# Performance work log

Measured on AMD Instinct MI355X. Metric: run time of the kernel, lower is better.

## Reference

```python
import jax, jax.numpy as jnp
import numpy as np

B, N, M = 16, 4096, 256
Q_DIM, CTX_DIM = 512, 768
HEADS, DIM_HEAD = 8, 64
INNER = HEADS * DIM_HEAD
SCALE = DIM_HEAD ** -0.5


def setup_inputs() -> dict:
    key = jax.random.key(0)
    ks = jax.random.split(key, 8)
    x = jax.random.normal(ks[0], (B, N, Q_DIM), dtype=jnp.float32)
    obj_txt = jax.random.normal(ks[1], (B, M, CTX_DIM), dtype=jnp.float32)
    obj_mask = jax.random.randint(ks[2], (B, N, M), 0, 2) > 0
    obj_vector = jnp.ones((B, M), dtype=bool)  # all-True keeps output finite (see notes)
    Wq = jax.random.normal(ks[3], (Q_DIM, INNER), dtype=jnp.float32) * 0.02
    Wk = jax.random.normal(ks[4], (CTX_DIM, INNER), dtype=jnp.float32) * 0.02
    Wv = jax.random.normal(ks[5], (CTX_DIM, INNER), dtype=jnp.float32) * 0.02
    Wo = jax.random.normal(ks[6], (INNER, Q_DIM), dtype=jnp.float32) * 0.02
    bo = jnp.zeros((Q_DIM,), dtype=jnp.float32)
    return {"x": x, "obj_txt": obj_txt, "obj_mask": obj_mask, "obj_vector": obj_vector,
            "Wq": Wq, "Wk": Wk, "Wv": Wv, "Wo": Wo, "bo": bo}


def reference(x, obj_txt, obj_mask, obj_vector, Wq, Wk, Wv, Wo, bo):
    b, n, _ = x.shape
    m = obj_txt.shape[1]
    q = (x @ Wq).reshape(b, n, HEADS, DIM_HEAD)          # [B,N,H,C]
    k = (obj_txt @ Wk).reshape(b, m, HEADS, DIM_HEAD)    # [B,M,H,C]
    v = (obj_txt @ Wv).reshape(b, m, HEADS, DIM_HEAD)
    sim = jnp.einsum('bnhc,bmhc->bhnm', q, k) * SCALE    # [B,H,N,M]
    neg = -jnp.finfo(sim.dtype).max
    # pre-softmax mask (obj_vector broadcasts over heads and queries)
    sim = jnp.where(obj_vector[:, None, None, :], sim, neg)
    # NOTE: original computes sim.softmax(-1) but then discards it, using the
    # pre-softmax masked sim with ~obj_mask positions set to 0 as the attention.
    attn = jnp.where(obj_mask[:, None, :, :], sim, jnp.array(0.0, sim.dtype))
    out = jnp.einsum('bhnm,bmhc->bnhc', attn, v).reshape(b, n, INNER)
    return out @ Wo + bo
```

## Files before the change

kernel.cpp:

```cpp
#include <hip/hip_runtime.h>

typedef unsigned short u16;
typedef unsigned char u8;
typedef unsigned int u32;
typedef unsigned long long u64;
typedef __attribute__((ext_vector_type(4))) float floatx4;
typedef __attribute__((ext_vector_type(8))) __bf16 bf16x8;

#define GLD_LDS(SRC, DST) __builtin_amdgcn_global_load_lds( \
    (const __attribute__((address_space(1))) void*)(SRC),   \
    (__attribute__((address_space(3))) void*)(DST), 16, 0, 0)

static __device__ __forceinline__ u16 f2bf(float f) {
  return __builtin_bit_cast(u16, (__bf16)f);
}
static __device__ __forceinline__ u32 pk2bf(float a, float b) {
  return (u32)f2bf(a) | ((u32)f2bf(b) << 16);
}
static __device__ __forceinline__ floatx4 mfma16(bf16x8 a, bf16x8 b, floatx4 c) {
  return __builtin_amdgcn_mfma_f32_16x16x32_bf16(a, b, c, 0, 0, 0);
}


__global__ void detect_mask_kernel(const unsigned int* __restrict__ m, int* __restrict__ flag) {
  __shared__ int sh[4];
  int t = threadIdx.x;
  int any = 0;
  for (int i = t; i < 16384; i += 256) any |= ((m[i] & 0xFFFFFF00u) != 0u) ? 1 : 0;
  unsigned long long b = __ballot(any != 0);
  if ((t & 63) == 0) sh[t >> 6] = (b != 0ull) ? 1 : 0;
  __syncthreads();
  if (t == 0) flag[0] = (sh[0] | sh[1] | sh[2] | sh[3]);
}

__global__ void prep_weights_kernel(const float* __restrict__ Wq, const float* __restrict__ Wk,
                                    const float* __restrict__ Wv, const float* __restrict__ Wo,
                                    u16* __restrict__ WqT, u16* __restrict__ WkT,
                                    u16* __restrict__ WvT, u16* __restrict__ WoT) {
  int z = blockIdx.y;
  const float* src = (z == 0) ? Wq : (z == 1) ? Wk : (z == 2) ? Wv : Wo;
  u16* dst = (z == 0) ? WqT : (z == 1) ? WkT : (z == 2) ? WvT : WoT;
  int K = (z == 1 || z == 2) ? 768 : 512;
  int total = K * 512;
  int idx = blockIdx.x * 256 + threadIdx.x;
  if (idx >= total) return;
  int n = idx / K, k = idx - n * K;
  float v = src[(size_t)k * 512 + n];
  if (z == 0) v *= 0.125f;
  dst[idx] = f2bf(v);
}

__global__ __launch_bounds__(256) void gemm_q_kernel(
    const float* __restrict__ A, const u16* __restrict__ Bt, u16* __restrict__ Cout) {
  __shared__ float Asf[2][4096];
  __shared__ u16 Bs[2][8192];
  int bid = blockIdx.x;
  int m0 = (bid >> 1) * 128, n0 = (bid & 1) * 256;
  int t = threadIdx.x, lane = t & 63;
  int w = t >> 6, wr = w >> 1, wc = w & 1, lr = lane & 15, lg = lane >> 4;
  floatx4 acc[4][8];
#pragma unroll
  for (int i = 0; i < 4; ++i)
#pragma unroll
    for (int j = 0; j < 8; ++j) acc[i][j] = (floatx4){0.f, 0.f, 0.f, 0.f};

  auto stage = [&](int kt, int bf) {
    int k0 = kt * 32;
#pragma unroll
    for (int i = 0; i < 4; ++i) {
      int idx = (i * 4 + w) * 64 + lane;
      int row = idx >> 3, g = idx & 7;
      int gs = g ^ (row & 7);
      const float* src = A + (size_t)(m0 + row) * 512 + k0 + gs * 4;
      char* dst = ((char*)&Asf[0][0]) + bf * 16384 + (i * 4 + w) * 1024;
      GLD_LDS(src, dst);
    }
#pragma unroll
    for (int i = 0; i < 4; ++i) {
      int idx = (i * 4 + w) * 64 + lane;
      int row = idx >> 2, g = idx & 3;
      int gs = g ^ ((row >> 1) & 3);
      const u16* src = Bt + (size_t)(n0 + row) * 512 + k0 + gs * 8;
      char* dst = ((char*)&Bs[0][0]) + bf * 16384 + (i * 4 + w) * 1024;
      GLD_LDS(src, dst);
    }
  };

  stage(0, 0);
  __syncthreads();
  for (int kt = 0; kt < 16; ++kt) {
    int cur = kt & 1;
    if (kt + 1 < 16) stage(kt + 1, cur ^ 1);
    bf16x8 av[4];
#pragma unroll
    for (int i = 0; i < 4; ++i) {
      int r = wr * 64 + i * 16 + lr;
      int g0 = (2 * lg) ^ (r & 7), g1 = (2 * lg + 1) ^ (r & 7);
      float4 f0 = *reinterpret_cast<const float4*>(&Asf[cur][r * 32 + g0 * 4]);
      float4 f1 = *reinterpret_cast<const float4*>(&Asf[cur][r * 32 + g1 * 4]);
      bf16x8 pk;
      pk[0] = (__bf16)f0.x; pk[1] = (__bf16)f0.y; pk[2] = (__bf16)f0.z; pk[3] = (__bf16)f0.w;
      pk[4] = (__bf16)f1.x; pk[5] = (__bf16)f1.y; pk[6] = (__bf16)f1.z; pk[7] = (__bf16)f1.w;
      av[i] = pk;
    }
#pragma unroll
    for (int j = 0; j < 8; ++j) {
      int rb = wc * 128 + j * 16 + lr;
      int gb = lg ^ ((rb >> 1) & 3);
      bf16x8 bv = *reinterpret_cast<const bf16x8*>(&Bs[cur][rb * 32 + gb * 8]);
#pragma unroll
      for (int i = 0; i < 4; ++i) acc[i][j] = mfma16(bv, av[i], acc[i][j]);
    }
    __syncthreads();
  }
#pragma unroll
  for (int i = 0; i < 4; ++i)
#pragma unroll
    for (int j = 0; j < 8; ++j) {
      int n_row = m0 + wr * 64 + i * 16 + lr;
      int colb = n0 + wc * 128 + j * 16 + lg * 4;
      ushort4 pk4;
      pk4.x = f2bf(acc[i][j][0]); pk4.y = f2bf(acc[i][j][1]);
      pk4.z = f2bf(acc[i][j][2]); pk4.w = f2bf(acc[i][j][3]);
      *reinterpret_cast<ushort4*>(&Cout[(size_t)n_row * 512 + colb]) = pk4;
    }
}

__global__ __launch_bounds__(256) void gemm_kv_kernel(
    const float* __restrict__ A, const u16* __restrict__ Bt0, const u16* __restrict__ Bt1,
    u16* __restrict__ C0, u16* __restrict__ C1) {
  const u16* Bt = Bt0;
  u16* Cout = C0;
  int mode = 0;
  if (blockIdx.z == 1) { Bt = Bt1; Cout = C1; mode = 2; }
  __shared__ float Asf[2][4096];
  __shared__ u16 Bs[2][4096];
  int m0 = blockIdx.x * 128, n0 = blockIdx.y * 128;
  int t = threadIdx.x, lane = t & 63;
  int w = t >> 6, wr = w >> 1, wc = w & 1, lr = lane & 15, lg = lane >> 4;
  floatx4 acc[4][4];
#pragma unroll
  for (int i = 0; i < 4; ++i)
#pragma unroll
    for (int j = 0; j < 4; ++j) acc[i][j] = (floatx4){0.f, 0.f, 0.f, 0.f};

  auto stage = [&](int kt, int bf) {
    int k0 = kt * 32;
#pragma unroll
    for (int i = 0; i < 4; ++i) {
      int idx = (i * 4 + w) * 64 + lane;
      int row = idx >> 3, g = idx & 7;
      int gs = g ^ (row & 7);
      const float* src = A + (size_t)(m0 + row) * 768 + k0 + gs * 4;
      char* dst = ((char*)&Asf[0][0]) + bf * 16384 + (i * 4 + w) * 1024;
      GLD_LDS(src, dst);
    }
#pragma unroll
    for (int i = 0; i < 2; ++i) {
      int idx = (i * 4 + w) * 64 + lane;
      int row = idx >> 2, g = idx & 3;
      int gs = g ^ ((row >> 1) & 3);
      const u16* src = Bt + (size_t)(n0 + row) * 768 + k0 + gs * 8;
      char* dst = ((char*)&Bs[0][0]) + bf * 8192 + (i * 4 + w) * 1024;
      GLD_LDS(src, dst);
    }
  };

  stage(0, 0);
  __syncthreads();
  for (int kt = 0; kt < 24; ++kt) {
    int cur = kt & 1;
    if (kt + 1 < 24) stage(kt + 1, cur ^ 1);
    bf16x8 av[4];
#pragma unroll
    for (int i = 0; i < 4; ++i) {
      int r = wr * 64 + i * 16 + lr;
      int g0 = (2 * lg) ^ (r & 7), g1 = (2 * lg + 1) ^ (r & 7);
      float4 f0 = *reinterpret_cast<const float4*>(&Asf[cur][r * 32 + g0 * 4]);
      float4 f1 = *reinterpret_cast<const float4*>(&Asf[cur][r * 32 + g1 * 4]);
      bf16x8 pk;
      pk[0] = (__bf16)f0.x; pk[1] = (__bf16)f0.y; pk[2] = (__bf16)f0.z; pk[3] = (__bf16)f0.w;
      pk[4] = (__bf16)f1.x; pk[5] = (__bf16)f1.y; pk[6] = (__bf16)f1.z; pk[7] = (__bf16)f1.w;
      av[i] = pk;
    }
#pragma unroll
    for (int j = 0; j < 4; ++j) {
      int rb = wc * 64 + j * 16 + lr;
      int gb = lg ^ ((rb >> 1) & 3);
      bf16x8 bv = *reinterpret_cast<const bf16x8*>(&Bs[cur][rb * 32 + gb * 8]);
#pragma unroll
      for (int i = 0; i < 4; ++i) acc[i][j] = mfma16(bv, av[i], acc[i][j]);
    }
    __syncthreads();
  }
#pragma unroll
  for (int i = 0; i < 4; ++i)
#pragma unroll
    for (int j = 0; j < 4; ++j) {
      int n_row = m0 + wr * 64 + i * 16 + lr;
      int colb = n0 + wc * 64 + j * 16 + lg * 4;
      if (mode == 0) {
        ushort4 pk4;
        pk4.x = f2bf(acc[i][j][0]); pk4.y = f2bf(acc[i][j][1]);
        pk4.z = f2bf(acc[i][j][2]); pk4.w = f2bf(acc[i][j][3]);
        *reinterpret_cast<ushort4*>(&Cout[(size_t)n_row * 512 + colb]) = pk4;
      } else {
        int bb = n_row >> 8, mm = n_row & 255;
#pragma unroll
        for (int r = 0; r < 4; ++r) {
          int col = colb + r;
          int hh = col >> 6, cc = col & 63;
          Cout[(((size_t)(bb * 8 + hh)) * 64 + cc) * 256 + mm] = f2bf(acc[i][j][r]);
        }
      }
    }
}

__global__ __launch_bounds__(256) void gemm_o_kernel(
    const u16* __restrict__ A, const u16* __restrict__ Bt, const float* __restrict__ bo,
    float* __restrict__ out) {
  __shared__ u16 As[2][4096];
  __shared__ u16 Bs[2][8192];
  int bid = blockIdx.x;
  int m0 = (bid >> 1) * 128, n0 = (bid & 1) * 256;
  int t = threadIdx.x, lane = t & 63;
  int w = t >> 6, wr = w >> 1, wc = w & 1, lr = lane & 15, lg = lane >> 4;
  floatx4 acc[4][8];
#pragma unroll
  for (int i = 0; i < 4; ++i)
#pragma unroll
    for (int j = 0; j < 8; ++j) acc[i][j] = (floatx4){0.f, 0.f, 0.f, 0.f};

  auto stage = [&](int kt, int bf) {
    int k0 = kt * 32;
#pragma unroll
    for (int i = 0; i < 2; ++i) {
      int idx = (i * 4 + w) * 64 + lane;
      int row = idx >> 2, g = idx & 3;
      int gs = g ^ ((row >> 1) & 3);
      const u16* src = A + (size_t)(m0 + row) * 512 + k0 + gs * 8;
      char* dst = ((char*)&As[0][0]) + bf * 8192 + (i * 4 + w) * 1024;
      GLD_LDS(src, dst);
    }
#pragma unroll
    for (int i = 0; i < 4; ++i) {
      int idx = (i * 4 + w) * 64 + lane;
      int row = idx >> 2, g = idx & 3;
      int gs = g ^ ((row >> 1) & 3);
      const u16* src = Bt + (size_t)(n0 + row) * 512 + k0 + gs * 8;
      char* dst = ((char*)&Bs[0][0]) + bf * 16384 + (i * 4 + w) * 1024;
      GLD_LDS(src, dst);
    }
  };

  stage(0, 0);
  __syncthreads();
  for (int kt = 0; kt < 16; ++kt) {
    int cur = kt & 1;
    if (kt + 1 < 16) stage(kt + 1, cur ^ 1);
    bf16x8 av[4];
#pragma unroll
    for (int i = 0; i < 4; ++i) {
      int r = wr * 64 + i * 16 + lr;
      int ga = lg ^ ((r >> 1) & 3);
      av[i] = *reinterpret_cast<const bf16x8*>(&As[cur][r * 32 + ga * 8]);
    }
#pragma unroll
    for (int j = 0; j < 8; ++j) {
      int rb = wc * 128 + j * 16 + lr;
      int gb = lg ^ ((rb >> 1) & 3);
      bf16x8 bv = *reinterpret_cast<const bf16x8*>(&Bs[cur][rb * 32 + gb * 8]);
#pragma unroll
      for (int i = 0; i < 4; ++i) acc[i][j] = mfma16(bv, av[i], acc[i][j]);
    }
    __syncthreads();
  }
#pragma unroll
  for (int i = 0; i < 4; ++i)
#pragma unroll
    for (int j = 0; j < 8; ++j) {
      int n_row = m0 + wr * 64 + i * 16 + lr;
      int colb = n0 + wc * 128 + j * 16 + lg * 4;
      float4 bv4 = *reinterpret_cast<const float4*>(&bo[colb]);
      float4 st;
      st.x = acc[i][j][0] + bv4.x; st.y = acc[i][j][1] + bv4.y;
      st.z = acc[i][j][2] + bv4.z; st.w = acc[i][j][3] + bv4.w;
      *reinterpret_cast<float4*>(&out[(size_t)n_row * 512 + colb]) = st;
    }
}

__global__ __launch_bounds__(512, 2) void attn_kernel(
    u16* qoin, const u16* __restrict__ Kb, const u16* __restrict__ Vt,
    const void* __restrict__ maskp, const int* __restrict__ flag) {
  __shared__ u16 k_lds[16384];
  __shared__ u16 v_lds[16384];
  __shared__ u16 ubuf[8][1024];
  int id = blockIdx.y * 32 + blockIdx.x;
  int xcd = id & 7, j0 = id >> 3;
  int bIdx = 2 * xcd + (j0 >> 5);
  int nx = j0 & 31;
  int lane = threadIdx.x & 63, w = threadIdx.x >> 6, lr = lane & 15, lg = lane >> 4;
  int n0w = nx * 128 + w * 16;
  bool mByte = flag[0] != 0;

  u64 mb;
  {
    int n = n0w + lr;
    size_t base = ((size_t)(bIdx * 4096 + n)) * 256;
    u64 bits = 0;
    if (mByte) {
      const u8* mp = (const u8*)maskp + base;
      for (int mt = 0; mt < 16; ++mt) {
        u32 dw = *(const u32*)(mp + mt * 16 + lg * 4);
#pragma unroll
        for (int r = 0; r < 4; ++r)
          if ((dw >> (8 * r)) & 0xFFu) bits |= (1ull << (mt * 4 + r));
      }
    } else {
      const int* mp = (const int*)maskp + base;
      for (int mt = 0; mt < 16; ++mt) {
        int4 q = *(const int4*)(mp + mt * 16 + lg * 4);
        if (q.x) bits |= 1ull << (mt * 4 + 0);
        if (q.y) bits |= 1ull << (mt * 4 + 1);
        if (q.z) bits |= 1ull << (mt * 4 + 2);
        if (q.w) bits |= 1ull << (mt * 4 + 3);
      }
    }
    mb = bits;
  }

  for (int h = 0; h < 8; ++h) {
    __syncthreads();
#pragma unroll
    for (int i = 0; i < 4; ++i) {
      int idx = (i * 8 + w) * 64 + lane;
      int m = idx >> 3, g = idx & 7;
      int gs = g ^ (m & 7);
      const u16* src = Kb + ((size_t)(bIdx * 256 + m)) * 512 + h * 64 + gs * 8;
      char* dst = ((char*)k_lds) + (i * 8 + w) * 1024;
      GLD_LDS(src, dst);
    }
#pragma unroll
    for (int i = 0; i < 4; ++i) {
      int idx = (i * 8 + w) * 64 + lane;
      int c = idx >> 5, g = idx & 31;
      int gs = (g & 24) | ((g & 7) ^ (c & 7));
      const u16* src = Vt + (((size_t)(bIdx * 8 + h)) * 64 + c) * 256 + gs * 8;
      char* dst = ((char*)v_lds) + (i * 8 + w) * 1024;
      GLD_LDS(src, dst);
    }
    bf16x8 qf[2];
#pragma unroll
    for (int ks = 0; ks < 2; ++ks)
      qf[ks] = *reinterpret_cast<const bf16x8*>(
          qoin + ((size_t)(bIdx * 4096 + n0w + lr)) * 512 + h * 64 + ks * 32 + lg * 8);
    __syncthreads();

    floatx4 acc2[4];
#pragma unroll
    for (int ct = 0; ct < 4; ++ct) acc2[ct] = (floatx4){0.f, 0.f, 0.f, 0.f};

    for (int ch = 0; ch < 8; ++ch) {
      floatx4 s[2];
#pragma unroll
      for (int mt2 = 0; mt2 < 2; ++mt2) s[mt2] = (floatx4){0.f, 0.f, 0.f, 0.f};
#pragma unroll
      for (int mt2 = 0; mt2 < 2; ++mt2) {
        int m = (ch * 2 + mt2) * 16 + lr;
#pragma unroll
        for (int ks = 0; ks < 2; ++ks) {
          int g = ks * 4 + lg;
          bf16x8 af = *reinterpret_cast<const bf16x8*>(&k_lds[m * 64 + ((g ^ (m & 7)) << 3)]);
          s[mt2] = mfma16(af, qf[ks], s[mt2]);
        }
      }
      u32* pb = (u32*)&ubuf[w][0];
#pragma unroll
      for (int mt2 = 0; mt2 < 2; ++mt2) {
        int sh = (ch * 2 + mt2) * 4;
        float v0 = ((mb >> (sh + 0)) & 1ull) ? s[mt2][0] : 0.f;
        float v1 = ((mb >> (sh + 1)) & 1ull) ? s[mt2][1] : 0.f;
        float v2 = ((mb >> (sh + 2)) & 1ull) ? s[mt2][2] : 0.f;
        float v3 = ((mb >> (sh + 3)) & 1ull) ? s[mt2][3] : 0.f;
        int gm = mt2 * 4 + lg;
        int gmp = gm ^ ((lr & 3) << 1);
        u64 pkd = (u64)pk2bf(v0, v1) | ((u64)pk2bf(v2, v3) << 32);
        *(u64*)(pb + lr * 16 + gmp * 2) = pkd;
      }
      int gmp = (2 * lg) ^ ((lr & 3) << 1);
      bf16x8 pf = *reinterpret_cast<const bf16x8*>(&ubuf[w][lr * 32 + gmp * 4]);
#pragma unroll
      for (int ct = 0; ct < 4; ++ct) {
        int c = ct * 16 + lr;
        int gv = ch * 4 + lg;
        int gvp = (gv & 24) | ((gv & 7) ^ (c & 7));
        bf16x8 vf = *reinterpret_cast<const bf16x8*>(&v_lds[c * 256 + gvp * 8]);
        acc2[ct] = mfma16(pf, vf, acc2[ct]);
      }
    }

#pragma unroll
    for (int ct = 0; ct < 4; ++ct)
#pragma unroll
      for (int r = 0; r < 4; ++r) {
        int c = ct * 16 + lr;
        int n = lg * 4 + r;
        int cg = c >> 3;
        ubuf[w][n * 64 + ((cg ^ (n & 7)) << 3) + (c & 7)] = f2bf(acc2[ct][r]);
      }
#pragma unroll
    for (int half = 0; half < 2; ++half) {
      int np = (lane >> 3) + half * 8;
      int cc = lane & 7;
      bf16x8 frag = *reinterpret_cast<const bf16x8*>(&ubuf[w][np * 64 + ((cc ^ (np & 7)) << 3)]);
      *reinterpret_cast<bf16x8*>(
          qoin + ((size_t)(bIdx * 4096 + n0w + np)) * 512 + h * 64 + cc * 8) = frag;
    }
  }
}

extern "C" void kernel_launch(void* const* d_in, const int* in_sizes, int n_in,
                              void* d_out, int out_size, void* d_ws, size_t ws_size,
                              hipStream_t stream) {
  const float* x = (const float*)d_in[0];
  const float* obj_txt = (const float*)d_in[1];
  const void* obj_mask = d_in[2];
  const float* Wq = (const float*)d_in[4];
  const float* Wk = (const float*)d_in[5];
  const float* Wv = (const float*)d_in[6];
  const float* Wo = (const float*)d_in[7];
  const float* bo = (const float*)d_in[8];
  float* out = (float*)d_out;

  char* ws = (char*)d_ws;
  u16* Qb = (u16*)ws;
  u16* Kb = (u16*)(ws + 67108864);
  u16* Vt = (u16*)(ws + 71303168);
  u16* WqT = (u16*)(ws + 75497472);
  u16* WkT = (u16*)(ws + 76021760);
  u16* WvT = (u16*)(ws + 76808192);
  u16* WoT = (u16*)(ws + 77594624);
  int* flag = (int*)(ws + 78118912);

  detect_mask_kernel<<<1, 256, 0, stream>>>((const unsigned int*)obj_mask, flag);
  prep_weights_kernel<<<dim3(1536, 4, 1), 256, 0, stream>>>(Wq, Wk, Wv, Wo, WqT, WkT, WvT, WoT);
  gemm_q_kernel<<<1024, 256, 0, stream>>>(x, WqT, Qb);
  gemm_kv_kernel<<<dim3(32, 4, 2), 256, 0, stream>>>(obj_txt, WkT, WvT, Kb, Vt);
  attn_kernel<<<dim3(32, 16, 1), 512, 0, stream>>>(Qb, Kb, Vt, obj_mask, flag);
  gemm_o_kernel<<<1024, 256, 0, stream>>>(Qb, WoT, bo, out);
}
```

Baseline: 304.4 us.

## Pre-convert x to bf16 in a separate pass and tile the weight transpose

Adds a kernel that converts x from fp32 to bf16 into the output buffer, which serves as scratch, so the Q GEMM streams half as many bytes into LDS and skips per-tile float-to-bf16 packing. The weight prep kernel now transposes through a padded shared-memory tile so both reads and writes are coalesced. The cost is one extra launch and a full extra read and write pass over x (fp32 in, bf16 out), and gemm_o must fully overwrite the output buffer afterwards.

```diff
diff --git a/kernel.cpp b/kernel.cpp
--- a/kernel.cpp
+++ b/kernel.cpp
@@ -33,26 +33,52 @@
   if (t == 0) flag[0] = (sh[0] | sh[1] | sh[2] | sh[3]);
 }
 
-__global__ void prep_weights_kernel(const float* __restrict__ Wq, const float* __restrict__ Wk,
-                                    const float* __restrict__ Wv, const float* __restrict__ Wo,
-                                    u16* __restrict__ WqT, u16* __restrict__ WkT,
-                                    u16* __restrict__ WvT, u16* __restrict__ WoT) {
+__global__ __launch_bounds__(256) void convert_x_kernel(const float* __restrict__ x,
+                                                        u16* __restrict__ xb) {
+  for (int u = blockIdx.x * 256 + threadIdx.x; u < 4194304; u += 524288) {
+    const float4* p = reinterpret_cast<const float4*>(x + (size_t)u * 8);
+    float4 f0 = p[0], f1 = p[1];
+    bf16x8 pk;
+    pk[0] = (__bf16)f0.x; pk[1] = (__bf16)f0.y; pk[2] = (__bf16)f0.z; pk[3] = (__bf16)f0.w;
+    pk[4] = (__bf16)f1.x; pk[5] = (__bf16)f1.y; pk[6] = (__bf16)f1.z; pk[7] = (__bf16)f1.w;
+    *reinterpret_cast<bf16x8*>(xb + (size_t)u * 8) = pk;
+  }
+}
+
+__global__ __launch_bounds__(256) void prep_weights_kernel(
+    const float* __restrict__ Wq, const float* __restrict__ Wk,
+    const float* __restrict__ Wv, const float* __restrict__ Wo,
+    u16* __restrict__ WqT, u16* __restrict__ WkT,
+    u16* __restrict__ WvT, u16* __restrict__ WoT) {
   int z = blockIdx.y;
   const float* src = (z == 0) ? Wq : (z == 1) ? Wk : (z == 2) ? Wv : Wo;
   u16* dst = (z == 0) ? WqT : (z == 1) ? WkT : (z == 2) ? WvT : WoT;
   int K = (z == 1 || z == 2) ? 768 : 512;
-  int total = K * 512;
-  int idx = blockIdx.x * 256 + threadIdx.x;
-  if (idx >= total) return;
-  int n = idx / K, k = idx - n * K;
-  float v = src[(size_t)k * 512 + n];
-  if (z == 0) v *= 0.125f;
-  dst[idx] = f2bf(v);
+  int nk64 = K >> 6;
+  int tile = blockIdx.x;
+  int kt = tile % nk64, ntile = tile / nk64;
+  if (ntile >= 8) return;
+  int k0 = kt * 64, n0 = ntile * 64;
+  float scale = (z == 0) ? 0.125f : 1.f;
+  __shared__ u16 sh[64 * 65];
+  int t = threadIdx.x;
+#pragma unroll
+  for (int i = 0; i < 16; ++i) {
+    int kk = i * 4 + (t >> 6), nn = t & 63;
+    float v = src[(size_t)(k0 + kk) * 512 + n0 + nn] * scale;
+    sh[kk * 65 + nn] = f2bf(v);
+  }
+  __syncthreads();
+#pragma unroll
+  for (int i = 0; i < 16; ++i) {
+    int nn = i * 4 + (t >> 6), kk = t & 63;
+    dst[(size_t)(n0 + nn) * K + k0 + kk] = sh[kk * 65 + nn];
+  }
 }
 
 __global__ __launch_bounds__(256) void gemm_q_kernel(
-    const float* __restrict__ A, const u16* __restrict__ Bt, u16* __restrict__ Cout) {
-  __shared__ float Asf[2][4096];
+    const u16* __restrict__ A, const u16* __restrict__ Bt, u16* __restrict__ Cout) {
+  __shared__ u16 As[2][4096];
   __shared__ u16 Bs[2][8192];
   int bid = blockIdx.x;
   int m0 = (bid >> 1) * 128, n0 = (bid & 1) * 256;
@@ -67,12 +93,12 @@
   auto stage = [&](int kt, int bf) {
     int k0 = kt * 32;
 #pragma unroll
-    for (int i = 0; i < 4; ++i) {
-      int idx = (i * 4 + w) * 64 + lane;
-      int row = idx >> 3, g = idx & 7;
-      int gs = g ^ (row & 7);
-      const float* src = A + (size_t)(m0 + row) * 512 + k0 + gs * 4;
-      char* dst = ((char*)&Asf[0][0]) + bf * 16384 + (i * 4 + w) * 1024;
+    for (int i = 0; i < 2; ++i) {
+      int idx = (i * 4 + w) * 64 + lane;
+      int row = idx >> 2, g = idx & 3;
+      int gs = g ^ ((row >> 1) & 3);
+      const u16* src = A + (size_t)(m0 + row) * 512 + k0 + gs * 8;
+      char* dst = ((char*)&As[0][0]) + bf * 8192 + (i * 4 + w) * 1024;
       GLD_LDS(src, dst);
     }
 #pragma unroll
@@ -95,13 +121,8 @@
 #pragma unroll
     for (int i = 0; i < 4; ++i) {
       int r = wr * 64 + i * 16 + lr;
-      int g0 = (2 * lg) ^ (r & 7), g1 = (2 * lg + 1) ^ (r & 7);
-      float4 f0 = *reinterpret_cast<const float4*>(&Asf[cur][r * 32 + g0 * 4]);
-      float4 f1 = *reinterpret_cast<const float4*>(&Asf[cur][r * 32 + g1 * 4]);
-      bf16x8 pk;
-      pk[0] = (__bf16)f0.x; pk[1] = (__bf16)f0.y; pk[2] = (__bf16)f0.z; pk[3] = (__bf16)f0.w;
-      pk[4] = (__bf16)f1.x; pk[5] = (__bf16)f1.y; pk[6] = (__bf16)f1.z; pk[7] = (__bf16)f1.w;
-      av[i] = pk;
+      int ga = lg ^ ((r >> 1) & 3);
+      av[i] = *reinterpret_cast<const bf16x8*>(&As[cur][r * 32 + ga * 8]);
     }
 #pragma unroll
     for (int j = 0; j < 8; ++j) {
@@ -441,10 +462,12 @@
   u16* WvT = (u16*)(ws + 76808192);
   u16* WoT = (u16*)(ws + 77594624);
   int* flag = (int*)(ws + 78118912);
+  u16* xb = (u16*)d_out;
 
   detect_mask_kernel<<<1, 256, 0, stream>>>((const unsigned int*)obj_mask, flag);
-  prep_weights_kernel<<<dim3(1536, 4, 1), 256, 0, stream>>>(Wq, Wk, Wv, Wo, WqT, WkT, WvT, WoT);
-  gemm_q_kernel<<<1024, 256, 0, stream>>>(x, WqT, Qb);
+  prep_weights_kernel<<<dim3(96, 4, 1), 256, 0, stream>>>(Wq, Wk, Wv, Wo, WqT, WkT, WvT, WoT);
+  convert_x_kernel<<<2048, 256, 0, stream>>>(x, xb);
+  gemm_q_kernel<<<1024, 256, 0, stream>>>(xb, WqT, Qb);
   gemm_kv_kernel<<<dim3(32, 4, 2), 256, 0, stream>>>(obj_txt, WkT, WvT, Kb, Vt);
   attn_kernel<<<dim3(32, 16, 1), 512, 0, stream>>>(Qb, Kb, Vt, obj_mask, flag);
   gemm_o_kernel<<<1024, 256, 0, stream>>>(Qb, WoT, bo, out);
```

Result: no change. 301.6 us (-0.9%).
